# Kernel optimization log

Measured on AMD Instinct MI355X. Metric: run time of the kernel, lower is better.

Reference implementation:

```python
import jax, jax.numpy as jnp
import numpy as np

HEADS = 2
NEG_SLOPE = 0.2  # PyG GATConv default leaky_relu slope


def gat_conv(x, edge_index, W, a_src, a_dst, bias, num_nodes):
    """PyG-style GATConv with concat=True and self-loops.
    x: [N, Fin], W: [Fin, H*C], a_src/a_dst: [H, C], bias: [H*C].
    edge_index: [2, E] with row 0 = source j, row 1 = target i.
    """
    H = HEADS
    C = W.shape[1] // H
    # add self loops
    loops = jnp.arange(num_nodes, dtype=edge_index.dtype)
    src = jnp.concatenate([edge_index[0], loops])
    dst = jnp.concatenate([edge_index[1], loops])

    xW = (x @ W).reshape(num_nodes, H, C)            # [N, H, C]
    alpha_s = jnp.einsum('nhc,hc->nh', xW, a_src)    # [N, H]
    alpha_d = jnp.einsum('nhc,hc->nh', xW, a_dst)    # [N, H]
    e = alpha_s[src] + alpha_d[dst]                  # [E, H]
    e = jax.nn.leaky_relu(e, NEG_SLOPE)
    # segment softmax over edges sharing the same target node
    m = jax.ops.segment_max(e, dst, num_segments=num_nodes)  # [N, H]
    e = jnp.exp(e - m[dst])
    denom = jax.ops.segment_sum(e, dst, num_segments=num_nodes)  # [N, H]
    alpha = e / denom[dst]                           # [E, H]
    # message = alpha_ij * xW_j, aggregated at target i
    msg = xW[src] * alpha[:, :, None]                # [E, H, C]
    out = jax.ops.segment_sum(msg, dst, num_segments=num_nodes)  # [N, H, C]
    return out.reshape(num_nodes, H * C) + bias


def setup_inputs() -> dict:
    key = jax.random.key(0)
    ks = jax.random.split(key, 10)
    N, E = 50000, 800000
    Fin, D = 128, 128
    H = HEADS
    x = jax.random.normal(ks[0], (N, Fin), dtype=jnp.float32)
    edge_index = jax.random.randint(ks[1], (2, E), 0, N, dtype=jnp.int64)
    g = 1.0 / np.sqrt(Fin)
    W1 = jax.random.normal(ks[2], (Fin, H * D), dtype=jnp.float32) * g
    a_src1 = jax.random.normal(ks[3], (H, D), dtype=jnp.float32) * g
    a_dst1 = jax.random.normal(ks[4], (H, D), dtype=jnp.float32) * g
    b1 = jnp.zeros((H * D,), dtype=jnp.float32)
    g2 = 1.0 / np.sqrt(H * D)
    W2 = jax.random.normal(ks[5], (H * D, H * D), dtype=jnp.float32) * g2
    a_src2 = jax.random.normal(ks[6], (H, D), dtype=jnp.float32) * g2
    a_dst2 = jax.random.normal(ks[7], (H, D), dtype=jnp.float32) * g2
    b2 = jnp.zeros((H * D,), dtype=jnp.float32)
    return {"x": x, "edge_index": edge_index,
            "W1": W1, "a_src1": a_src1, "a_dst1": a_dst1, "b1": b1,
            "W2": W2, "a_src2": a_src2, "a_dst2": a_dst2, "b2": b2}


def reference(x, edge_index, W1, a_src1, a_dst1, b1, W2, a_src2, a_dst2, b2):
    N = x.shape[0]
    h = gat_conv(x, edge_index, W1, a_src1, a_dst1, b1, N)
    h = jax.nn.elu(h)
    # dropout is identity in eval mode (deterministic reference)
    out = gat_conv(h, edge_index, W2, a_src2, a_dst2, b2, N)
    return out
```

## Files before the change

### kernel.cpp

```cpp
#include <hip/hip_runtime.h>
#include <math.h>

#define HEADS 2
#define CH    128
#define HC    256
#define NEG   0.2f

typedef __attribute__((ext_vector_type(8))) short  bfrag8;
typedef __attribute__((ext_vector_type(4))) float  f32x4;

__device__ inline unsigned short f2bf_rne(float x) {
    unsigned u = __float_as_uint(x);
    u += 0x7fffu + ((u >> 16) & 1u);
    return (unsigned short)(u >> 16);
}

__global__ __launch_bounds__(256)
void prep_w_kernel(const float* __restrict__ W1, const float* __restrict__ W2,
                   unsigned short* __restrict__ wt1, unsigned short* __restrict__ wt2,
                   int K1) {
    int idx = blockIdx.x * 256 + threadIdx.x;
    const int n1 = K1 * HC;
    if (idx < n1) {
        const int k = idx >> 8, n = idx & 255;
        wt1[(size_t)n * K1 + k] = f2bf_rne(W1[idx]);
    } else {
        idx -= n1;
        if (idx < HC * HC) {
            const int k = idx >> 8, n = idx & 255;
            wt2[(size_t)n * HC + k] = f2bf_rne(W2[idx]);
        }
    }
}

__device__ inline void va_row(const float* __restrict__ W, const float* __restrict__ a_src,
                              const float* __restrict__ a_dst, float* __restrict__ va,
                              int k, int lane) {
    const int c0 = lane * 4;
    const float4 w4 = *reinterpret_cast<const float4*>(&W[(size_t)k * HC + c0]);
    const float4 s4 = *reinterpret_cast<const float4*>(&a_src[c0]);
    const float4 d4 = *reinterpret_cast<const float4*>(&a_dst[c0]);
    float ps = w4.x * s4.x + w4.y * s4.y + w4.z * s4.z + w4.w * s4.w;
    float pd = w4.x * d4.x + w4.y * d4.y + w4.z * d4.z + w4.w * d4.w;
    #pragma unroll
    for (int m = 1; m <= 16; m <<= 1) {
        ps += __shfl_xor(ps, m);
        pd += __shfl_xor(pd, m);
    }
    if (lane == 0)  { va[k * 4 + 0] = ps; va[k * 4 + 2] = pd; }
    if (lane == 32) { va[k * 4 + 1] = ps; va[k * 4 + 3] = pd; }
}

__global__ __launch_bounds__(256)
void prep_va_kernel(const float* __restrict__ W1, const float* __restrict__ as1,
                    const float* __restrict__ ad1, float* __restrict__ va1,
                    const float* __restrict__ W2, const float* __restrict__ as2,
                    const float* __restrict__ ad2, float* __restrict__ va2, int K1) {
    int g = (blockIdx.x * 256 + threadIdx.x) >> 6;
    const int lane = threadIdx.x & 63;
    if (g < K1)           va_row(W1, as1, ad1, va1, g, lane);
    else { g -= K1; if (g < HC) va_row(W2, as2, ad2, va2, g, lane); }
}

__global__ __launch_bounds__(256)
void xprep_hist_kernel(const float* __restrict__ x, const float* __restrict__ va,
                       unsigned short* __restrict__ xb, float* __restrict__ as_out,
                       float* __restrict__ ad_out, int N, int K,
                       const int* __restrict__ dst, int* __restrict__ counts,
                       int E, int nxp) {
    if ((int)blockIdx.x >= nxp) {
        const int e = ((int)blockIdx.x - nxp) * 256 + threadIdx.x;
        if (e < E) atomicAdd(&counts[dst[e]], 1);
        return;
    }
    const int i    = (blockIdx.x * 256 + threadIdx.x) >> 6;
    const int lane = threadIdx.x & 63;
    if (i >= N) return;
    const float2 v = reinterpret_cast<const float2*>(&x[(size_t)i * K])[lane];
    ushort2 bv; bv.x = f2bf_rne(v.x); bv.y = f2bf_rne(v.y);
    reinterpret_cast<ushort2*>(&xb[(size_t)i * K])[lane] = bv;

    const float4 a0 = reinterpret_cast<const float4*>(va)[lane * 2 + 0];
    const float4 a1 = reinterpret_cast<const float4*>(va)[lane * 2 + 1];
    float p0 = v.x * a0.x + v.y * a1.x;
    float p1 = v.x * a0.y + v.y * a1.y;
    float p2 = v.x * a0.z + v.y * a1.z;
    float p3 = v.x * a0.w + v.y * a1.w;
    #pragma unroll
    for (int m = 1; m <= 32; m <<= 1) {
        p0 += __shfl_xor(p0, m);
        p1 += __shfl_xor(p1, m);
        p2 += __shfl_xor(p2, m);
        p3 += __shfl_xor(p3, m);
    }
    if (lane == 0) {
        as_out[i * 2 + 0] = p0; as_out[i * 2 + 1] = p1;
        ad_out[i * 2 + 0] = p2; ad_out[i * 2 + 1] = p3;
    }
}

__global__ __launch_bounds__(256)
void hlogit_kernel(const unsigned short* __restrict__ hb, const float* __restrict__ va,
                   float* __restrict__ as2, float* __restrict__ ad2, int N) {
    const int i    = (blockIdx.x * 256 + threadIdx.x) >> 6;
    const int lane = threadIdx.x & 63;
    if (i >= N) return;
    const uint2 q = reinterpret_cast<const uint2*>(&hb[(size_t)i * HC])[lane];
    float f[4];
    f[0] = __uint_as_float(q.x << 16);
    f[1] = __uint_as_float(q.x & 0xffff0000u);
    f[2] = __uint_as_float(q.y << 16);
    f[3] = __uint_as_float(q.y & 0xffff0000u);
    float p0 = 0.f, p1 = 0.f, p2 = 0.f, p3 = 0.f;
    #pragma unroll
    for (int r = 0; r < 4; ++r) {
        const float4 vv = reinterpret_cast<const float4*>(va)[lane * 4 + r];
        p0 = fmaf(f[r], vv.x, p0);
        p1 = fmaf(f[r], vv.y, p1);
        p2 = fmaf(f[r], vv.z, p2);
        p3 = fmaf(f[r], vv.w, p3);
    }
    #pragma unroll
    for (int m = 1; m <= 32; m <<= 1) {
        p0 += __shfl_xor(p0, m);
        p1 += __shfl_xor(p1, m);
        p2 += __shfl_xor(p2, m);
        p3 += __shfl_xor(p3, m);
    }
    if (lane == 0) {
        as2[i * 2 + 0] = p0; as2[i * 2 + 1] = p1;
        ad2[i * 2 + 0] = p2; ad2[i * 2 + 1] = p3;
    }
}

__global__ __launch_bounds__(256)
void gemm_msg_kernel(const unsigned short* __restrict__ Ab,
                     const unsigned short* __restrict__ Wt,
                     unsigned short* __restrict__ xWb, int M, int K) {
    __shared__ unsigned short Ah[128][72];
    __shared__ unsigned short Bh[128][72];

    const int t    = threadIdx.x;
    const int row0 = blockIdx.x * 128;
    const int col0 = blockIdx.y * 128;
    const int lane = t & 63;
    const int wid  = t >> 6;
    const int wr   = wid >> 1;
    const int wc   = wid & 1;

    f32x4 acc[4][4] = {};

    const int arow = t & 127;
    const int aseg = (t >> 7) * 32;

    for (int kk = 0; kk < K; kk += 64) {
        {
            const int gr = row0 + arow;
            #pragma unroll
            for (int q = 0; q < 4; ++q) {
                bfrag8 v = {0,0,0,0,0,0,0,0};
                if (gr < M)
                    v = *reinterpret_cast<const bfrag8*>(&Ab[(size_t)gr * K + kk + aseg + q * 8]);
                *reinterpret_cast<bfrag8*>(&Ah[arow][aseg + q * 8]) = v;
            }
            #pragma unroll
            for (int q = 0; q < 4; ++q) {
                const bfrag8 w = *reinterpret_cast<const bfrag8*>(
                    &Wt[(size_t)(col0 + arow) * K + kk + aseg + q * 8]);
                *reinterpret_cast<bfrag8*>(&Bh[arow][aseg + q * 8]) = w;
            }
        }
        __syncthreads();

        const int ko = (lane >> 4) * 8;
        #pragma unroll
        for (int kb = 0; kb < 64; kb += 32) {
            bfrag8 ah[4], bh[4];
            #pragma unroll
            for (int m = 0; m < 4; ++m)
                ah[m] = *reinterpret_cast<const bfrag8*>(&Ah[wr * 64 + m * 16 + (lane & 15)][kb + ko]);
            #pragma unroll
            for (int n = 0; n < 4; ++n)
                bh[n] = *reinterpret_cast<const bfrag8*>(&Bh[wc * 64 + n * 16 + (lane & 15)][kb + ko]);
            #pragma unroll
            for (int m = 0; m < 4; ++m)
                #pragma unroll
                for (int n = 0; n < 4; ++n)
                    acc[m][n] = __builtin_amdgcn_mfma_f32_16x16x32_bf16(ah[m], bh[n], acc[m][n], 0, 0, 0);
        }
        __syncthreads();
    }

    #pragma unroll
    for (int m = 0; m < 4; ++m) {
        #pragma unroll
        for (int reg = 0; reg < 4; ++reg) {
            const int gr = row0 + wr * 64 + m * 16 + (lane >> 4) * 4 + reg;
            if (gr < M) {
                unsigned short* rp = &xWb[(size_t)gr * HC + col0];
                #pragma unroll
                for (int n = 0; n < 4; ++n)
                    rp[wc * 64 + n * 16 + (lane & 15)] = f2bf_rne(acc[m][n][reg]);
            }
        }
    }
}

__global__ __launch_bounds__(256)
void scan_local_kernel(int* __restrict__ data, int* __restrict__ chunk_sum, int N) {
    __shared__ int s[256];
    const int t   = threadIdx.x;
    const int idx = blockIdx.x * 256 + t;
    const int v   = (idx < N) ? data[idx] : 0;
    s[t] = v;
    __syncthreads();
    #pragma unroll
    for (int off = 1; off < 256; off <<= 1) {
        int x = (t >= off) ? s[t - off] : 0;
        __syncthreads();
        s[t] += x;
        __syncthreads();
    }
    if (idx < N) data[idx] = s[t] - v;
    if (t == 255) chunk_sum[blockIdx.x] = s[255];
}

__global__ __launch_bounds__(256)
void scan_chunks_kernel(int* __restrict__ chunk, int nb) {
    __shared__ int s[256];
    const int t = threadIdx.x;
    const int v = (t < nb) ? chunk[t] : 0;
    s[t] = v;
    __syncthreads();
    #pragma unroll
    for (int off = 1; off < 256; off <<= 1) {
        int x = (t >= off) ? s[t - off] : 0;
        __syncthreads();
        s[t] += x;
        __syncthreads();
    }
    if (t < nb) chunk[t] = s[t] - v;
}

__global__ __launch_bounds__(256)
void add_offsets_kernel(const int* __restrict__ excl, const int* __restrict__ chunk_excl,
                        int* __restrict__ row_ptr, int* __restrict__ cursor,
                        int N, int E) {
    const int idx = blockIdx.x * 256 + threadIdx.x;
    if (idx < N) {
        const int rp = excl[idx] + chunk_excl[idx >> 8];
        row_ptr[idx] = rp;
        cursor[idx]  = rp;
    }
    if (idx == 0) row_ptr[N] = E;
}

__global__ __launch_bounds__(256)
void scatter_kernel(const int* __restrict__ src, const int* __restrict__ dst,
                    int* __restrict__ cursor, int* __restrict__ col_idx, int E) {
    const int e = blockIdx.x * 256 + threadIdx.x;
    if (e < E) {
        const int pos = atomicAdd(&cursor[dst[e]], 1);
        col_idx[pos] = src[e];
    }
}

__global__ __launch_bounds__(256)
void agg_kernel(const int* __restrict__ row_ptr, const int* __restrict__ col_idx,
                const unsigned short* __restrict__ xWb,
                const float* __restrict__ as_, const float* __restrict__ ad_,
                const float* __restrict__ bias, float* __restrict__ outf,
                unsigned short* __restrict__ hb, int N, int mode) {
    const int wv   = (blockIdx.x * 256 + threadIdx.x) >> 6;
    const int lane = threadIdx.x & 63;
    if (wv >= N) return;
    const int i    = wv;
    const int half = lane >> 5;
    const int sl   = lane & 31;
    const int hh   = sl >> 4;
    const int cb   = hh * 128 + (sl & 15) * 8;
    const float adi = ad_[i * 2 + hh];

    float acc[8] = {};
    float dn = 0.f;

    const int beg = row_ptr[i];
    const int end = row_ptr[i + 1];

    int k = beg + half;
    int j = (k < end) ? col_idx[k] : 0;
    for (; k < end; k += 2) {
        const int jn = (k + 2 < end) ? col_idx[k + 2] : 0;
        float e = as_[j * 2 + hh] + adi;
        e = e > 0.f ? e : NEG * e;
        const float w = expf(e);
        const uint4 q = *reinterpret_cast<const uint4*>(&xWb[(size_t)j * HC + cb]);
        const unsigned qq[4] = {q.x, q.y, q.z, q.w};
        #pragma unroll
        for (int r = 0; r < 4; ++r) {
            const float flo = __uint_as_float(qq[r] << 16);
            const float fhi = __uint_as_float(qq[r] & 0xffff0000u);
            acc[r * 2 + 0] = fmaf(w, flo, acc[r * 2 + 0]);
            acc[r * 2 + 1] = fmaf(w, fhi, acc[r * 2 + 1]);
        }
        dn += w;
        j = jn;
    }

    #pragma unroll
    for (int r = 0; r < 8; ++r) acc[r] += __shfl_xor(acc[r], 32);
    dn += __shfl_xor(dn, 32);

    if (lane < 32) {
        float e = as_[i * 2 + hh] + adi;
        e = e > 0.f ? e : NEG * e;
        const float ws = expf(e);
        const uint4 q = *reinterpret_cast<const uint4*>(&xWb[(size_t)i * HC + cb]);
        const unsigned qq[4] = {q.x, q.y, q.z, q.w};
        #pragma unroll
        for (int r = 0; r < 4; ++r) {
            const float flo = __uint_as_float(qq[r] << 16);
            const float fhi = __uint_as_float(qq[r] & 0xffff0000u);
            acc[r * 2 + 0] = fmaf(ws, flo, acc[r * 2 + 0]);
            acc[r * 2 + 1] = fmaf(ws, fhi, acc[r * 2 + 1]);
        }
        dn += ws;

        const float inv = 1.f / dn;
        const float4 b0 = *reinterpret_cast<const float4*>(&bias[cb]);
        const float4 b1 = *reinterpret_cast<const float4*>(&bias[cb + 4]);
        float o[8];
        o[0] = acc[0] * inv + b0.x; o[1] = acc[1] * inv + b0.y;
        o[2] = acc[2] * inv + b0.z; o[3] = acc[3] * inv + b0.w;
        o[4] = acc[4] * inv + b1.x; o[5] = acc[5] * inv + b1.y;
        o[6] = acc[6] * inv + b1.z; o[7] = acc[7] * inv + b1.w;

        if (mode) {
            #pragma unroll
            for (int r = 0; r < 8; ++r) o[r] = o[r] > 0.f ? o[r] : expm1f(o[r]);
            bfrag8 hv;
            #pragma unroll
            for (int r = 0; r < 8; ++r) hv[r] = (short)f2bf_rne(o[r]);
            *reinterpret_cast<bfrag8*>(&hb[(size_t)i * HC + cb]) = hv;
        } else {
            *reinterpret_cast<float4*>(&outf[(size_t)i * HC + cb]) =
                make_float4(o[0], o[1], o[2], o[3]);
            *reinterpret_cast<float4*>(&outf[(size_t)i * HC + cb + 4]) =
                make_float4(o[4], o[5], o[6], o[7]);
        }
    }
}

extern "C" void kernel_launch(void* const* d_in, const int* in_sizes, int n_in,
                              void* d_out, int out_size, void* d_ws, size_t ws_size,
                              hipStream_t stream) {
    const float* x      = (const float*)d_in[0];
    const int*   ei     = (const int*)d_in[1];
    const float* W1     = (const float*)d_in[2];
    const float* a_src1 = (const float*)d_in[3];
    const float* a_dst1 = (const float*)d_in[4];
    const float* b1     = (const float*)d_in[5];
    const float* W2     = (const float*)d_in[6];
    const float* a_src2 = (const float*)d_in[7];
    const float* a_dst2 = (const float*)d_in[8];
    const float* b2     = (const float*)d_in[9];
    float* out = (float*)d_out;

    const int Nn = in_sizes[0] / 128;
    const int E  = in_sizes[1] / 2;
    const int K1 = in_sizes[2] / HC;
    const int* src = ei;
    const int* dst = ei + E;

    float* as1   = (float*)d_ws;
    float* ad1   = as1 + (size_t)Nn * 2;
    float* as2   = ad1 + (size_t)Nn * 2;
    float* ad2   = as2 + (size_t)Nn * 2;
    float* va1   = ad2 + (size_t)Nn * 2;
    float* va2   = va1 + (size_t)K1 * 4;
    int*   tmp   = (int*)(va2 + (size_t)HC * 4);
    int*   chunk = tmp + Nn;
    int*   rowp  = chunk + 256;
    int*   curs  = rowp + (Nn + 1);
    int*   colx  = curs + Nn;
    uintptr_t pa = ((uintptr_t)(colx + E) + 31) & ~(uintptr_t)31;
    unsigned short* wt1 = (unsigned short*)pa;
    unsigned short* wt2 = wt1 + (size_t)HC * K1;
    unsigned short* xb  = wt2 + (size_t)HC * HC;
    unsigned short* xWb = xb  + (size_t)Nn * K1;
    unsigned short* hb  = xWb + (size_t)Nn * HC;

    const int nb  = (Nn + 255) / 256;
    const int nxp = (Nn + 3) / 4;
    const int nhb = (E + 255) / 256;

    hipMemsetAsync(tmp, 0, (size_t)Nn * sizeof(int), stream);
    prep_w_kernel<<<(K1 * HC + HC * HC + 255) / 256, 256, 0, stream>>>(W1, W2, wt1, wt2, K1);
    prep_va_kernel<<<(K1 + HC + 3) / 4, 256, 0, stream>>>(W1, a_src1, a_dst1, va1,
                                                          W2, a_src2, a_dst2, va2, K1);
    xprep_hist_kernel<<<nxp + nhb, 256, 0, stream>>>(x, va1, xb, as1, ad1, Nn, K1,
                                                     dst, tmp, E, nxp);
    scan_local_kernel<<<nb, 256, 0, stream>>>(tmp, chunk, Nn);
    scan_chunks_kernel<<<1, 256, 0, stream>>>(chunk, nb);
    add_offsets_kernel<<<nb, 256, 0, stream>>>(tmp, chunk, rowp, curs, Nn, E);
    scatter_kernel<<<nhb, 256, 0, stream>>>(src, dst, curs, colx, E);

    const dim3 ggrid((Nn + 127) / 128, HC / 128);
    const int  agrid = (Nn + 3) / 4;

    gemm_msg_kernel<<<ggrid, 256, 0, stream>>>(xb, wt1, xWb, Nn, K1);
    agg_kernel<<<agrid, 256, 0, stream>>>(rowp, colx, xWb, as1, ad1, b1,
                                          (float*)nullptr, hb, Nn, 1);
    hlogit_kernel<<<agrid, 256, 0, stream>>>(hb, va2, as2, ad2, Nn);

    gemm_msg_kernel<<<ggrid, 256, 0, stream>>>(hb, wt2, xWb, Nn, HC);
    agg_kernel<<<agrid, 256, 0, stream>>>(rowp, colx, xWb, as2, ad2, b2,
                                          out, (unsigned short*)nullptr, Nn, 0);
}
```

Measured before the change: 339.7 us.

## Merge independent kernels to cut launch count and serialization

Independent preprocessing stages are merged into single launches. Weight conversion joins the x-prep/histogram kernel. The chunk scan and offset add are fused, with each block reducing its own prefix of chunk sums. The CSR scatter shares a launch with the first GEMM, and the layer-2 logit computation shares a launch with the second GEMM. This removes several launches and their serialization gaps so the small tasks can overlap with the GEMMs, at the cost of heterogeneous blocks and redundant per-block prefix reductions.

```diff
diff --git a/kernel.cpp b/kernel.cpp
--- a/kernel.cpp
+++ b/kernel.cpp
@@ -13,24 +13,6 @@
     unsigned u = __float_as_uint(x);
     u += 0x7fffu + ((u >> 16) & 1u);
     return (unsigned short)(u >> 16);
-}
-
-__global__ __launch_bounds__(256)
-void prep_w_kernel(const float* __restrict__ W1, const float* __restrict__ W2,
-                   unsigned short* __restrict__ wt1, unsigned short* __restrict__ wt2,
-                   int K1) {
-    int idx = blockIdx.x * 256 + threadIdx.x;
-    const int n1 = K1 * HC;
-    if (idx < n1) {
-        const int k = idx >> 8, n = idx & 255;
-        wt1[(size_t)n * K1 + k] = f2bf_rne(W1[idx]);
-    } else {
-        idx -= n1;
-        if (idx < HC * HC) {
-            const int k = idx >> 8, n = idx & 255;
-            wt2[(size_t)n * HC + k] = f2bf_rne(W2[idx]);
-        }
-    }
 }
 
 __device__ inline void va_row(const float* __restrict__ W, const float* __restrict__ a_src,
@@ -63,147 +45,58 @@
 }
 
 __global__ __launch_bounds__(256)
-void xprep_hist_kernel(const float* __restrict__ x, const float* __restrict__ va,
-                       unsigned short* __restrict__ xb, float* __restrict__ as_out,
-                       float* __restrict__ ad_out, int N, int K,
-                       const int* __restrict__ dst, int* __restrict__ counts,
-                       int E, int nxp) {
-    if ((int)blockIdx.x >= nxp) {
-        const int e = ((int)blockIdx.x - nxp) * 256 + threadIdx.x;
-        if (e < E) atomicAdd(&counts[dst[e]], 1);
+void prep_big_kernel(const float* __restrict__ W1, const float* __restrict__ W2,
+                     unsigned short* __restrict__ wt1, unsigned short* __restrict__ wt2,
+                     const float* __restrict__ x, const float* __restrict__ va,
+                     unsigned short* __restrict__ xb, float* __restrict__ as_out,
+                     float* __restrict__ ad_out,
+                     const int* __restrict__ dst, int* __restrict__ counts,
+                     int N, int K1, int E, int nW, int nxp) {
+    const int bx = (int)blockIdx.x;
+    if (bx < nW) {
+        int idx = bx * 256 + threadIdx.x;
+        const int n1 = K1 * HC;
+        if (idx < n1) {
+            const int k = idx >> 8, n = idx & 255;
+            wt1[(size_t)n * K1 + k] = f2bf_rne(W1[idx]);
+        } else {
+            idx -= n1;
+            if (idx < HC * HC) {
+                const int k = idx >> 8, n = idx & 255;
+                wt2[(size_t)n * HC + k] = f2bf_rne(W2[idx]);
+            }
+        }
         return;
     }
-    const int i    = (blockIdx.x * 256 + threadIdx.x) >> 6;
-    const int lane = threadIdx.x & 63;
-    if (i >= N) return;
-    const float2 v = reinterpret_cast<const float2*>(&x[(size_t)i * K])[lane];
-    ushort2 bv; bv.x = f2bf_rne(v.x); bv.y = f2bf_rne(v.y);
-    reinterpret_cast<ushort2*>(&xb[(size_t)i * K])[lane] = bv;
-
-    const float4 a0 = reinterpret_cast<const float4*>(va)[lane * 2 + 0];
-    const float4 a1 = reinterpret_cast<const float4*>(va)[lane * 2 + 1];
-    float p0 = v.x * a0.x + v.y * a1.x;
-    float p1 = v.x * a0.y + v.y * a1.y;
-    float p2 = v.x * a0.z + v.y * a1.z;
-    float p3 = v.x * a0.w + v.y * a1.w;
-    #pragma unroll
-    for (int m = 1; m <= 32; m <<= 1) {
-        p0 += __shfl_xor(p0, m);
-        p1 += __shfl_xor(p1, m);
-        p2 += __shfl_xor(p2, m);
-        p3 += __shfl_xor(p3, m);
-    }
-    if (lane == 0) {
-        as_out[i * 2 + 0] = p0; as_out[i * 2 + 1] = p1;
-        ad_out[i * 2 + 0] = p2; ad_out[i * 2 + 1] = p3;
-    }
-}
-
-__global__ __launch_bounds__(256)
-void hlogit_kernel(const unsigned short* __restrict__ hb, const float* __restrict__ va,
-                   float* __restrict__ as2, float* __restrict__ ad2, int N) {
-    const int i    = (blockIdx.x * 256 + threadIdx.x) >> 6;
-    const int lane = threadIdx.x & 63;
-    if (i >= N) return;
-    const uint2 q = reinterpret_cast<const uint2*>(&hb[(size_t)i * HC])[lane];
-    float f[4];
-    f[0] = __uint_as_float(q.x << 16);
-    f[1] = __uint_as_float(q.x & 0xffff0000u);
-    f[2] = __uint_as_float(q.y << 16);
-    f[3] = __uint_as_float(q.y & 0xffff0000u);
-    float p0 = 0.f, p1 = 0.f, p2 = 0.f, p3 = 0.f;
-    #pragma unroll
-    for (int r = 0; r < 4; ++r) {
-        const float4 vv = reinterpret_cast<const float4*>(va)[lane * 4 + r];
-        p0 = fmaf(f[r], vv.x, p0);
-        p1 = fmaf(f[r], vv.y, p1);
-        p2 = fmaf(f[r], vv.z, p2);
-        p3 = fmaf(f[r], vv.w, p3);
-    }
-    #pragma unroll
-    for (int m = 1; m <= 32; m <<= 1) {
-        p0 += __shfl_xor(p0, m);
-        p1 += __shfl_xor(p1, m);
-        p2 += __shfl_xor(p2, m);
-        p3 += __shfl_xor(p3, m);
-    }
-    if (lane == 0) {
-        as2[i * 2 + 0] = p0; as2[i * 2 + 1] = p1;
-        ad2[i * 2 + 0] = p2; ad2[i * 2 + 1] = p3;
-    }
-}
-
-__global__ __launch_bounds__(256)
-void gemm_msg_kernel(const unsigned short* __restrict__ Ab,
-                     const unsigned short* __restrict__ Wt,
-                     unsigned short* __restrict__ xWb, int M, int K) {
-    __shared__ unsigned short Ah[128][72];
-    __shared__ unsigned short Bh[128][72];
-
-    const int t    = threadIdx.x;
-    const int row0 = blockIdx.x * 128;
-    const int col0 = blockIdx.y * 128;
-    const int lane = t & 63;
-    const int wid  = t >> 6;
-    const int wr   = wid >> 1;
-    const int wc   = wid & 1;
-
-    f32x4 acc[4][4] = {};
-
-    const int arow = t & 127;
-    const int aseg = (t >> 7) * 32;
-
-    for (int kk = 0; kk < K; kk += 64) {
-        {
-            const int gr = row0 + arow;
-            #pragma unroll
-            for (int q = 0; q < 4; ++q) {
-                bfrag8 v = {0,0,0,0,0,0,0,0};
-                if (gr < M)
-                    v = *reinterpret_cast<const bfrag8*>(&Ab[(size_t)gr * K + kk + aseg + q * 8]);
-                *reinterpret_cast<bfrag8*>(&Ah[arow][aseg + q * 8]) = v;
-            }
-            #pragma unroll
-            for (int q = 0; q < 4; ++q) {
-                const bfrag8 w = *reinterpret_cast<const bfrag8*>(
-                    &Wt[(size_t)(col0 + arow) * K + kk + aseg + q * 8]);
-                *reinterpret_cast<bfrag8*>(&Bh[arow][aseg + q * 8]) = w;
-            }
-        }
-        __syncthreads();
-
-        const int ko = (lane >> 4) * 8;
-        #pragma unroll
-        for (int kb = 0; kb < 64; kb += 32) {
-            bfrag8 ah[4], bh[4];
-            #pragma unroll
-            for (int m = 0; m < 4; ++m)
-                ah[m] = *reinterpret_cast<const bfrag8*>(&Ah[wr * 64 + m * 16 + (lane & 15)][kb + ko]);
-            #pragma unroll
-            for (int n = 0; n < 4; ++n)
-                bh[n] = *reinterpret_cast<const bfrag8*>(&Bh[wc * 64 + n * 16 + (lane & 15)][kb + ko]);
-            #pragma unroll
-            for (int m = 0; m < 4; ++m)
-                #pragma unroll
-                for (int n = 0; n < 4; ++n)
-                    acc[m][n] = __builtin_amdgcn_mfma_f32_16x16x32_bf16(ah[m], bh[n], acc[m][n], 0, 0, 0);
-        }
-        __syncthreads();
-    }
-
-    #pragma unroll
-    for (int m = 0; m < 4; ++m) {
-        #pragma unroll
-        for (int reg = 0; reg < 4; ++reg) {
-            const int gr = row0 + wr * 64 + m * 16 + (lane >> 4) * 4 + reg;
-            if (gr < M) {
-                unsigned short* rp = &xWb[(size_t)gr * HC + col0];
-                #pragma unroll
-                for (int n = 0; n < 4; ++n)
-                    rp[wc * 64 + n * 16 + (lane & 15)] = f2bf_rne(acc[m][n][reg]);
-            }
-        }
-    }
+    if (bx < nW + nxp) {
+        const int i    = ((bx - nW) * 256 + threadIdx.x) >> 6;
+        const int lane = threadIdx.x & 63;
+        if (i >= N) return;
+        const float2 v = reinterpret_cast<const float2*>(&x[(size_t)i * K1])[lane];
+        ushort2 bv; bv.x = f2bf_rne(v.x); bv.y = f2bf_rne(v.y);
+        reinterpret_cast<ushort2*>(&xb[(size_t)i * K1])[lane] = bv;
+
+        const float4 a0 = reinterpret_cast<const float4*>(va)[lane * 2 + 0];
+        const float4 a1 = reinterpret_cast<const float4*>(va)[lane * 2 + 1];
+        float p0 = v.x * a0.x + v.y * a1.x;
+        float p1 = v.x * a0.y + v.y * a1.y;
+        float p2 = v.x * a0.z + v.y * a1.z;
+        float p3 = v.x * a0.w + v.y * a1.w;
+        #pragma unroll
+        for (int m = 1; m <= 32; m <<= 1) {
+            p0 += __shfl_xor(p0, m);
+            p1 += __shfl_xor(p1, m);
+            p2 += __shfl_xor(p2, m);
+            p3 += __shfl_xor(p3, m);
+        }
+        if (lane == 0) {
+            as_out[i * 2 + 0] = p0; as_out[i * 2 + 1] = p1;
+            ad_out[i * 2 + 0] = p2; ad_out[i * 2 + 1] = p3;
+        }
+        return;
+    }
+    const int e = (bx - nW - nxp) * 256 + threadIdx.x;
+    if (e < E) atomicAdd(&counts[dst[e]], 1);
 }
 
 __global__ __launch_bounds__(256)
@@ -226,43 +119,164 @@
 }
 
 __global__ __launch_bounds__(256)
-void scan_chunks_kernel(int* __restrict__ chunk, int nb) {
+void offsets_kernel(const int* __restrict__ excl, const int* __restrict__ chunk_sum,
+                    int* __restrict__ row_ptr, int* __restrict__ cursor,
+                    int N, int E, int nb) {
     __shared__ int s[256];
-    const int t = threadIdx.x;
-    const int v = (t < nb) ? chunk[t] : 0;
-    s[t] = v;
+    const int t   = threadIdx.x;
+    const int bid = blockIdx.x;
+    s[t] = (t < bid && t < nb) ? chunk_sum[t] : 0;
     __syncthreads();
     #pragma unroll
-    for (int off = 1; off < 256; off <<= 1) {
-        int x = (t >= off) ? s[t - off] : 0;
+    for (int off = 128; off >= 1; off >>= 1) {
+        if (t < off) s[t] += s[t + off];
         __syncthreads();
-        s[t] += x;
-        __syncthreads();
-    }
-    if (t < nb) chunk[t] = s[t] - v;
-}
-
-__global__ __launch_bounds__(256)
-void add_offsets_kernel(const int* __restrict__ excl, const int* __restrict__ chunk_excl,
-                        int* __restrict__ row_ptr, int* __restrict__ cursor,
-                        int N, int E) {
-    const int idx = blockIdx.x * 256 + threadIdx.x;
+    }
+    const int base = s[0];
+    const int idx  = bid * 256 + t;
     if (idx < N) {
-        const int rp = excl[idx] + chunk_excl[idx >> 8];
+        const int rp = excl[idx] + base;
         row_ptr[idx] = rp;
         cursor[idx]  = rp;
     }
     if (idx == 0) row_ptr[N] = E;
 }
 
-__global__ __launch_bounds__(256)
-void scatter_kernel(const int* __restrict__ src, const int* __restrict__ dst,
-                    int* __restrict__ cursor, int* __restrict__ col_idx, int E) {
-    const int e = blockIdx.x * 256 + threadIdx.x;
-    if (e < E) {
-        const int pos = atomicAdd(&cursor[dst[e]], 1);
-        col_idx[pos] = src[e];
-    }
+__device__ inline void gemm_tile(const unsigned short* __restrict__ Ab,
+                                 const unsigned short* __restrict__ Wt,
+                                 unsigned short* __restrict__ xWb, int M, int K,
+                                 int bm, int bn,
+                                 unsigned short (*Ah)[72], unsigned short (*Bh)[72]) {
+    const int t    = threadIdx.x;
+    const int row0 = bm * 128;
+    const int col0 = bn * 128;
+    const int lane = t & 63;
+    const int wid  = t >> 6;
+    const int wr   = wid >> 1;
+    const int wc   = wid & 1;
+
+    f32x4 acc[4][4] = {};
+
+    const int arow = t & 127;
+    const int aseg = (t >> 7) * 32;
+
+    for (int kk = 0; kk < K; kk += 64) {
+        {
+            const int gr = row0 + arow;
+            #pragma unroll
+            for (int q = 0; q < 4; ++q) {
+                bfrag8 v = {0,0,0,0,0,0,0,0};
+                if (gr < M)
+                    v = *reinterpret_cast<const bfrag8*>(&Ab[(size_t)gr * K + kk + aseg + q * 8]);
+                *reinterpret_cast<bfrag8*>(&Ah[arow][aseg + q * 8]) = v;
+            }
+            #pragma unroll
+            for (int q = 0; q < 4; ++q) {
+                const bfrag8 w = *reinterpret_cast<const bfrag8*>(
+                    &Wt[(size_t)(col0 + arow) * K + kk + aseg + q * 8]);
+                *reinterpret_cast<bfrag8*>(&Bh[arow][aseg + q * 8]) = w;
+            }
+        }
+        __syncthreads();
+
+        const int ko = (lane >> 4) * 8;
+        #pragma unroll
+        for (int kb = 0; kb < 64; kb += 32) {
+            bfrag8 ah[4], bh[4];
+            #pragma unroll
+            for (int m = 0; m < 4; ++m)
+                ah[m] = *reinterpret_cast<const bfrag8*>(&Ah[wr * 64 + m * 16 + (lane & 15)][kb + ko]);
+            #pragma unroll
+            for (int n = 0; n < 4; ++n)
+                bh[n] = *reinterpret_cast<const bfrag8*>(&Bh[wc * 64 + n * 16 + (lane & 15)][kb + ko]);
+            #pragma unroll
+            for (int m = 0; m < 4; ++m)
+                #pragma unroll
+                for (int n = 0; n < 4; ++n)
+                    acc[m][n] = __builtin_amdgcn_mfma_f32_16x16x32_bf16(ah[m], bh[n], acc[m][n], 0, 0, 0);
+        }
+        __syncthreads();
+    }
+
+    #pragma unroll
+    for (int m = 0; m < 4; ++m) {
+        #pragma unroll
+        for (int reg = 0; reg < 4; ++reg) {
+            const int gr = row0 + wr * 64 + m * 16 + (lane >> 4) * 4 + reg;
+            if (gr < M) {
+                unsigned short* rp = &xWb[(size_t)gr * HC + col0];
+                #pragma unroll
+                for (int n = 0; n < 4; ++n)
+                    rp[wc * 64 + n * 16 + (lane & 15)] = f2bf_rne(acc[m][n][reg]);
+            }
+        }
+    }
+}
+
+__global__ __launch_bounds__(256)
+void gemm1_scatter_kernel(const unsigned short* __restrict__ Ab,
+                          const unsigned short* __restrict__ Wt,
+                          unsigned short* __restrict__ xWb, int M, int K,
+                          const int* __restrict__ src, const int* __restrict__ dst,
+                          int* __restrict__ cursor, int* __restrict__ col_idx,
+                          int E, int ngemm, int mtiles) {
+    __shared__ unsigned short Ah[128][72];
+    __shared__ unsigned short Bh[128][72];
+    const int bx = (int)blockIdx.x;
+    if (bx >= ngemm) {
+        const int e = (bx - ngemm) * 256 + threadIdx.x;
+        if (e < E) {
+            const int pos = atomicAdd(&cursor[dst[e]], 1);
+            col_idx[pos] = src[e];
+        }
+        return;
+    }
+    gemm_tile(Ab, Wt, xWb, M, K, bx % mtiles, bx / mtiles, Ah, Bh);
+}
+
+__global__ __launch_bounds__(256)
+void gemm2_hlogit_kernel(const unsigned short* __restrict__ hb,
+                         const unsigned short* __restrict__ Wt,
+                         unsigned short* __restrict__ xWb, int M, int K,
+                         const float* __restrict__ va,
+                         float* __restrict__ as2, float* __restrict__ ad2,
+                         int N, int ngemm, int mtiles) {
+    __shared__ unsigned short Ah[128][72];
+    __shared__ unsigned short Bh[128][72];
+    const int bx = (int)blockIdx.x;
+    if (bx >= ngemm) {
+        const int i    = ((bx - ngemm) * 256 + threadIdx.x) >> 6;
+        const int lane = threadIdx.x & 63;
+        if (i >= N) return;
+        const uint2 q = reinterpret_cast<const uint2*>(&hb[(size_t)i * HC])[lane];
+        float f[4];
+        f[0] = __uint_as_float(q.x << 16);
+        f[1] = __uint_as_float(q.x & 0xffff0000u);
+        f[2] = __uint_as_float(q.y << 16);
+        f[3] = __uint_as_float(q.y & 0xffff0000u);
+        float p0 = 0.f, p1 = 0.f, p2 = 0.f, p3 = 0.f;
+        #pragma unroll
+        for (int r = 0; r < 4; ++r) {
+            const float4 vv = reinterpret_cast<const float4*>(va)[lane * 4 + r];
+            p0 = fmaf(f[r], vv.x, p0);
+            p1 = fmaf(f[r], vv.y, p1);
+            p2 = fmaf(f[r], vv.z, p2);
+            p3 = fmaf(f[r], vv.w, p3);
+        }
+        #pragma unroll
+        for (int m = 1; m <= 32; m <<= 1) {
+            p0 += __shfl_xor(p0, m);
+            p1 += __shfl_xor(p1, m);
+            p2 += __shfl_xor(p2, m);
+            p3 += __shfl_xor(p3, m);
+        }
+        if (lane == 0) {
+            as2[i * 2 + 0] = p0; as2[i * 2 + 1] = p1;
+            ad2[i * 2 + 0] = p2; ad2[i * 2 + 1] = p3;
+        }
+        return;
+    }
+    gemm_tile(hb, Wt, xWb, M, K, bx % mtiles, bx / mtiles, Ah, Bh);
 }
 
 __global__ __launch_bounds__(256)
@@ -393,27 +407,27 @@
     const int nb  = (Nn + 255) / 256;
     const int nxp = (Nn + 3) / 4;
     const int nhb = (E + 255) / 256;
+    const int nW  = (K1 * HC + HC * HC + 255) / 256;
+    const int mt1 = (Nn + 127) / 128;
+    const int ng  = mt1 * (HC / 128);
+    const int agrid = nxp;
 
     hipMemsetAsync(tmp, 0, (size_t)Nn * sizeof(int), stream);
-    prep_w_kernel<<<(K1 * HC + HC * HC + 255) / 256, 256, 0, stream>>>(W1, W2, wt1, wt2, K1);
     prep_va_kernel<<<(K1 + HC + 3) / 4, 256, 0, stream>>>(W1, a_src1, a_dst1, va1,
                                                           W2, a_src2, a_dst2, va2, K1);
-    xprep_hist_kernel<<<nxp + nhb, 256, 0, stream>>>(x, va1, xb, as1, ad1, Nn, K1,
-                                                     dst, tmp, E, nxp);
+    prep_big_kernel<<<nW + nxp + nhb, 256, 0, stream>>>(W1, W2, wt1, wt2,
+                                                        x, va1, xb, as1, ad1,
+                                                        dst, tmp, Nn, K1, E, nW, nxp);
     scan_local_kernel<<<nb, 256, 0, stream>>>(tmp, chunk, Nn);
-    scan_chunks_kernel<<<1, 256, 0, stream>>>(chunk, nb);
-    add_offsets_kernel<<<nb, 256, 0, stream>>>(tmp, chunk, rowp, curs, Nn, E);
-    scatter_kernel<<<nhb, 256, 0, stream>>>(src, dst, curs, colx, E);
-
-    const dim3 ggrid((Nn + 127) / 128, HC / 128);
-    const int  agrid = (Nn + 3) / 4;
-
-    gemm_msg_kernel<<<ggrid, 256, 0, stream>>>(xb, wt1, xWb, Nn, K1);
+    offsets_kernel<<<nb, 256, 0, stream>>>(tmp, chunk, rowp, curs, Nn, E, nb);
+
+    gemm1_scatter_kernel<<<ng + nhb, 256, 0, stream>>>(xb, wt1, xWb, Nn, K1,
+                                                       src, dst, curs, colx, E, ng, mt1);
     agg_kernel<<<agrid, 256, 0, stream>>>(rowp, colx, xWb, as1, ad1, b1,
                                           (float*)nullptr, hb, Nn, 1);
-    hlogit_kernel<<<agrid, 256, 0, stream>>>(hb, va2, as2, ad2, Nn);
-
-    gemm_msg_kernel<<<ggrid, 256, 0, stream>>>(hb, wt2, xWb, Nn, HC);
+
+    gemm2_hlogit_kernel<<<ng + agrid, 256, 0, stream>>>(hb, wt2, xWb, Nn, HC,
+                                                        va2, as2, ad2, Nn, ng, mt1);
     agg_kernel<<<agrid, 256, 0, stream>>>(rowp, colx, xWb, as2, ad2, b2,
                                           out, (unsigned short*)nullptr, Nn, 0);
 }
```

Result: faster. 325.8 us, median of 2 (-4.1%).
